# Kernel optimization log

Measured on AMD Instinct MI355X. Metric: run time of the kernel, lower is better.

## Reference

```python
import jax, jax.numpy as jnp
import numpy as np

SLIDING_WINDOW = 512
LOGIT_SOFTCAP = 50.0
NEG_INF = -1e30


def setup_inputs() -> dict:
    key = jax.random.key(0)
    ks = jax.random.split(key, 3)
    B, S, H, KVH, D, BS = 4, 1024, 32, 8, 128, 64
    nb = S // BS          # blocks per sequence = 16
    nblocks = B * nb      # total cache blocks = 64
    total = B * S         # flattened tokens = 4096
    return {
        "query": jax.random.normal(ks[0], (total, H, D), dtype=jnp.float32),
        "key": jax.random.normal(ks[1], (total, KVH, D), dtype=jnp.float32),
        "value": jax.random.normal(ks[2], (total, KVH, D), dtype=jnp.float32),
        "k_cache": jnp.zeros((nblocks, BS, KVH, D), dtype=jnp.float32),
        "v_cache": jnp.zeros((nblocks, BS, KVH, D), dtype=jnp.float32),
        "block_offsets": jnp.arange(nblocks, dtype=jnp.int32).reshape(B, nb),
    }


def reference(query, key, value, k_cache, v_cache, block_offsets):
    B, nb = block_offsets.shape
    nblocks, BS, KVH, D = k_cache.shape
    S = nb * BS
    H = query.shape[1]
    G = H // KVH  # GQA group size
    scale = D ** -0.5

    flat_blocks = block_offsets.reshape(-1)  # [B*nb]
    # 1) write new keys/values into the paged cache per the block table
    k_cache = k_cache.at[flat_blocks].set(key.reshape(-1, BS, KVH, D))
    v_cache = v_cache.at[flat_blocks].set(value.reshape(-1, BS, KVH, D))
    # 2) gather per-sequence contiguous K/V from cache blocks
    k = k_cache[flat_blocks].reshape(B, S, KVH, D)
    v = v_cache[flat_blocks].reshape(B, S, KVH, D)

    q = query.reshape(B, S, KVH, G, D)
    scores = jnp.einsum("bqhgd,bkhd->bhgqk", q, k) * scale
    # logit softcapping (Gemma-style)
    scores = jnp.tanh(scores / LOGIT_SOFTCAP) * LOGIT_SOFTCAP
    # causal + sliding-window mask
    i = jnp.arange(S)[:, None]
    j = jnp.arange(S)[None, :]
    mask = (j <= i) & ((i - j) < SLIDING_WINDOW)
    scores = jnp.where(mask, scores, NEG_INF)
    p = jax.nn.softmax(scores, axis=-1)
    out = jnp.einsum("bhgqk,bkhd->bqhgd", p, v)
    return out.reshape(B * S, H, D)
```

## Files before the change

kernel.cpp:

```cpp
#include <hip/hip_runtime.h>
#include <hip/hip_bf16.h>

typedef __bf16 bf16_t;
typedef bf16_t bf16x8 __attribute__((ext_vector_type(8)));
typedef bf16_t bf16x4 __attribute__((ext_vector_type(4)));
typedef float f32x4 __attribute__((ext_vector_type(4)));

#define B_   4
#define S_   1024
#define H_   32
#define KVH_ 8
#define D_   128
#define WIN_ 512
#define KVD_ (KVH_ * D_)
#define LOG2E_ 1.4426950408889634f
#define C1_ (2.0f * (0.08838834764831845f / 50.0f) * LOG2E_)
#define K2_ (50.0f * LOG2E_)
#define EXP2F_(x) __builtin_amdgcn_exp2f(x)

__device__ __forceinline__ void async16(const bf16_t* g, bf16_t* l) {
  __builtin_amdgcn_global_load_lds(
      (const __attribute__((address_space(1))) void*)g,
      (__attribute__((address_space(3))) void*)l, 16, 0, 0);
}

__global__ __launch_bounds__(256) void prep_kv(
    const float* __restrict__ K, const float* __restrict__ V,
    bf16_t* __restrict__ Kb, bf16_t* __restrict__ Vt)
{
  const int j0  = blockIdx.x * 64;
  const int kvh = blockIdx.y;
  const int b   = blockIdx.z;
  const int t   = threadIdx.x;
  const int j   = t >> 2;
  const int d0  = (t & 3) * 32;
  __shared__ bf16_t tl[128][72];

  {
    const float* src = K + (size_t)(b * S_ + j0 + j) * KVD_ + kvh * D_ + d0;
    bf16_t* dst = Kb + ((size_t)(b * KVH_ + kvh) * S_ + j0 + j) * D_ + d0;
    #pragma unroll
    for (int c = 0; c < 4; ++c) {
      float4 f0 = *(const float4*)(src + c * 8);
      float4 f1 = *(const float4*)(src + c * 8 + 4);
      bf16x8 o = { (bf16_t)f0.x, (bf16_t)f0.y, (bf16_t)f0.z, (bf16_t)f0.w,
                   (bf16_t)f1.x, (bf16_t)f1.y, (bf16_t)f1.z, (bf16_t)f1.w };
      *(bf16x8*)(dst + c * 8) = o;
    }
  }
  {
    const float* src = V + (size_t)(b * S_ + j0 + j) * KVD_ + kvh * D_ + d0;
    #pragma unroll
    for (int c = 0; c < 8; ++c) {
      float4 f = *(const float4*)(src + c * 4);
      tl[d0 + c * 4 + 0][j] = (bf16_t)f.x;
      tl[d0 + c * 4 + 1][j] = (bf16_t)f.y;
      tl[d0 + c * 4 + 2][j] = (bf16_t)f.z;
      tl[d0 + c * 4 + 3][j] = (bf16_t)f.w;
    }
  }
  __syncthreads();
  {
    const int d = t >> 1, half = (t & 1) * 32;
    bf16_t* dst = Vt + ((size_t)(b * KVH_ + kvh) * D_ + d) * S_ + j0 + half;
    #pragma unroll
    for (int c = 0; c < 4; ++c)
      *(bf16x8*)(dst + c * 8) = *(bf16x8*)&tl[d][half + c * 8];
  }
}

__global__ __launch_bounds__(512, 2) void attn_fwd(
    const float* __restrict__ Q, const bf16_t* __restrict__ Kb,
    const bf16_t* __restrict__ Vt, float* __restrict__ Out)
{
  const int i0  = blockIdx.x * 32;
  const int kvh = blockIdx.y;
  const int b   = blockIdx.z;

  const int tid  = threadIdx.x;
  const int w    = tid >> 6;
  const int lane = tid & 63;
  const int m16  = lane & 15;
  const int quad = lane >> 4;
  const int g    = w & 3;
  const int rb   = w >> 2;
  const int h    = kvh * 4 + g;
  const int iw   = i0 + rb * 16;
  const int i    = iw + m16;

  __shared__ __align__(16) bf16_t KsB[2][64 * 128];
  __shared__ __align__(16) bf16_t VtB[2][128 * 64];
  __shared__ __align__(16) bf16_t PsB[8 * 16 * 64];

  bf16x8 qf[4];
  {
    const float* qp = Q + ((size_t)(b * S_ + iw + m16) * H_ + h) * D_;
    #pragma unroll
    for (int s = 0; s < 4; ++s) {
      const int d0 = 32 * s + 8 * quad;
      float4 f0 = *(const float4*)(qp + d0);
      float4 f1 = *(const float4*)(qp + d0 + 4);
      bf16x8 t = { (bf16_t)f0.x, (bf16_t)f0.y, (bf16_t)f0.z, (bf16_t)f0.w,
                   (bf16_t)f1.x, (bf16_t)f1.y, (bf16_t)f1.z, (bf16_t)f1.w };
      qf[s] = t;
    }
  }

  f32x4 O[8];
  #pragma unroll
  for (int c = 0; c < 8; ++c) O[c] = (f32x4){0.f, 0.f, 0.f, 0.f};
  float m_run = -1e30f, l_run = 0.f;

  const bf16_t* khead = Kb + (size_t)(b * KVH_ + kvh) * S_ * D_;
  const bf16_t* vhead = Vt + (size_t)(b * KVH_ + kvh) * D_ * S_;

  const int t_lo = (i0 >= WIN_) ? ((i0 - (WIN_ - 1)) >> 6) : 0;
  const int t_hi = i0 >> 6;

  auto stage = [&](int j0v, int bi) {
    #pragma unroll
    for (int q = 0; q < 2; ++q) {
      const int c   = w * 128 + q * 64 + lane;
      const int krow = c >> 4, kpos = c & 15;
      async16(khead + (size_t)(j0v + krow) * D_ + (((kpos ^ (krow & 15))) << 3),
              &KsB[bi][(w * 128 + q * 64) * 8]);
      const int vd = c >> 3, vpos = c & 7;
      async16(vhead + (size_t)vd * S_ + j0v + (((vpos ^ (vd & 7))) << 3),
              &VtB[bi][(w * 128 + q * 64) * 8]);
    }
  };

  stage(t_lo * 64, 0);
  int buf = 0;

  for (int tb = t_lo; tb <= t_hi; ++tb) {
    const int j0 = tb * 64;
    __syncthreads();
    if (tb < t_hi) stage(j0 + 64, buf ^ 1);

    if (!(j0 > iw + 15 || j0 + 63 < iw - (WIN_ - 1))) {
      f32x4 st[4];
      #pragma unroll
      for (int t4 = 0; t4 < 4; ++t4) {
        f32x4 acc = (f32x4){0.f, 0.f, 0.f, 0.f};
        const int row = 16 * t4 + m16;
        #pragma unroll
        for (int s = 0; s < 4; ++s) {
          bf16x8 a = *(const bf16x8*)&KsB[buf][row * 128 + (((quad + 4 * s) ^ m16) << 3)];
          acc = __builtin_amdgcn_mfma_f32_16x16x32_bf16(a, qf[s], acc, 0, 0, 0);
        }
        st[t4] = acc;
      }

      const bool full = (j0 + 63 <= iw) && (iw + 15 - j0 < WIN_);
      float vmax = -1e30f;
      if (full) {
        #pragma unroll
        for (int t4 = 0; t4 < 4; ++t4)
          #pragma unroll
          for (int r = 0; r < 4; ++r) {
            float ez  = EXP2F_(st[t4][r] * C1_);
            float cap = K2_ * (ez - 1.f) * __builtin_amdgcn_rcpf(ez + 1.f);
            st[t4][r] = cap;
            vmax = fmaxf(vmax, cap);
          }
      } else {
        #pragma unroll
        for (int t4 = 0; t4 < 4; ++t4)
          #pragma unroll
          for (int r = 0; r < 4; ++r) {
            const int j = j0 + t4 * 16 + 4 * quad + r;
            const bool valid = (j <= i) && (i - j < WIN_);
            float ez  = EXP2F_(st[t4][r] * C1_);
            float cap = K2_ * (ez - 1.f) * __builtin_amdgcn_rcpf(ez + 1.f);
            float sm  = valid ? cap : -1e30f;
            st[t4][r] = sm;
            vmax = fmaxf(vmax, sm);
          }
      }
      vmax = fmaxf(vmax, __shfl_xor(vmax, 16));
      vmax = fmaxf(vmax, __shfl_xor(vmax, 32));
      const float m_new = fmaxf(m_run, vmax);
      const float alpha = EXP2F_(m_run - m_new);

      float rs = 0.f;
      if (full) {
        #pragma unroll
        for (int t4 = 0; t4 < 4; ++t4)
          #pragma unroll
          for (int r = 0; r < 4; ++r) {
            float p = EXP2F_(st[t4][r] - m_new);
            st[t4][r] = p; rs += p;
          }
      } else {
        #pragma unroll
        for (int t4 = 0; t4 < 4; ++t4)
          #pragma unroll
          for (int r = 0; r < 4; ++r) {
            const int j = j0 + t4 * 16 + 4 * quad + r;
            const bool valid = (j <= i) && (i - j < WIN_);
            float p = valid ? EXP2F_(st[t4][r] - m_new) : 0.f;
            st[t4][r] = p; rs += p;
          }
      }
      rs += __shfl_xor(rs, 16);
      rs += __shfl_xor(rs, 32);
      l_run = l_run * alpha + rs;
      m_run = m_new;

      const int pw = w * (16 * 64);
      #pragma unroll
      for (int t4 = 0; t4 < 4; ++t4) {
        bf16x4 pk = { (bf16_t)st[t4][0], (bf16_t)st[t4][1],
                      (bf16_t)st[t4][2], (bf16_t)st[t4][3] };
        const int ch = (2 * t4 + (quad >> 1)) ^ (m16 & 7);
        *(bf16x4*)&PsB[pw + m16 * 64 + ch * 8 + (quad & 1) * 4] = pk;
      }
      bf16x8 pa0 = *(const bf16x8*)&PsB[pw + m16 * 64 + (((quad)     ^ (m16 & 7)) << 3)];
      bf16x8 pa1 = *(const bf16x8*)&PsB[pw + m16 * 64 + (((quad + 4) ^ (m16 & 7)) << 3)];

      if (__ballot(alpha != 1.0f)) {
        #pragma unroll
        for (int r = 0; r < 4; ++r) {
          const float ar = __shfl(alpha, 4 * quad + r);
          #pragma unroll
          for (int c = 0; c < 8; ++c) O[c][r] *= ar;
        }
      }

      #pragma unroll
      for (int c = 0; c < 8; ++c) {
        const int row = (16 * c + m16) * 64;
        bf16x8 v0 = *(const bf16x8*)&VtB[buf][row + (((quad)     ^ (m16 & 7)) << 3)];
        bf16x8 v1 = *(const bf16x8*)&VtB[buf][row + (((quad + 4) ^ (m16 & 7)) << 3)];
        O[c] = __builtin_amdgcn_mfma_f32_16x16x32_bf16(pa0, v0, O[c], 0, 0, 0);
        O[c] = __builtin_amdgcn_mfma_f32_16x16x32_bf16(pa1, v1, O[c], 0, 0, 0);
      }
    }
    buf ^= 1;
  }

  float* ob = Out + ((size_t)(b * S_ + iw) * H_ + h) * D_;
  #pragma unroll
  for (int r = 0; r < 4; ++r) {
    const int rr = 4 * quad + r;
    const float lr = __shfl(l_run, rr);
    const float linv = __builtin_amdgcn_rcpf(lr);
    float* po = ob + (size_t)rr * (H_ * D_);
    #pragma unroll
    for (int c = 0; c < 8; ++c) po[c * 16 + m16] = O[c][r] * linv;
  }
}

extern "C" void kernel_launch(void* const* d_in, const int* in_sizes, int n_in,
                              void* d_out, int out_size, void* d_ws, size_t ws_size,
                              hipStream_t stream) {
  const float* q = (const float*)d_in[0];
  const float* k = (const float*)d_in[1];
  const float* v = (const float*)d_in[2];
  float* out = (float*)d_out;
  const size_t nkv = (size_t)B_ * KVH_ * S_ * D_;
  bf16_t *kb, *vt;
  if (ws_size >= 2 * nkv * sizeof(bf16_t)) {
    kb = (bf16_t*)d_ws; vt = kb + nkv;
  } else {
    kb = (bf16_t*)d_in[3]; vt = (bf16_t*)d_in[4];
  }
  prep_kv<<<dim3(S_ / 64, KVH_, B_), 256, 0, stream>>>(k, v, kb, vt);
  attn_fwd<<<dim3(S_ / 32, KVH_, B_), 512, 0, stream>>>(q, kb, vt, out);
}
```

Measured before the change: 257.0 us.

## Drop online softmax max tracking using softcap bound; shrink KV tile to 32

Because softcapping bounds every score to at most 50, the kernel drops the running max, rescaling and the shuffle reductions. It computes p = exp(cap - 50) directly as exp2(-2*K2/(e+1)), which folds the tanh into a single exponential. The KV tile shrinks from 64 to 32 rows and staging moves from async global-to-LDS loads to register prefetch plus an LDS store. Launch bounds go to 6 blocks and a block-index swizzle groups tiles. The fixed offset gives up the numerical safety of the running max, though the bounded range keeps it stable, and the smaller tiles double the number of loop iterations and barriers.

```diff
diff --git a/kernel.cpp b/kernel.cpp
--- a/kernel.cpp
+++ b/kernel.cpp
@@ -16,13 +16,8 @@
 #define LOG2E_ 1.4426950408889634f
 #define C1_ (2.0f * (0.08838834764831845f / 50.0f) * LOG2E_)
 #define K2_ (50.0f * LOG2E_)
+#define NK22_ (-2.0f * K2_)
 #define EXP2F_(x) __builtin_amdgcn_exp2f(x)
-
-__device__ __forceinline__ void async16(const bf16_t* g, bf16_t* l) {
-  __builtin_amdgcn_global_load_lds(
-      (const __attribute__((address_space(1))) void*)g,
-      (__attribute__((address_space(3))) void*)l, 16, 0, 0);
-}
 
 __global__ __launch_bounds__(256) void prep_kv(
     const float* __restrict__ K, const float* __restrict__ V,
@@ -69,13 +64,15 @@
   }
 }
 
-__global__ __launch_bounds__(512, 2) void attn_fwd(
+__global__ __launch_bounds__(512, 6) void attn_fwd(
     const float* __restrict__ Q, const bf16_t* __restrict__ Kb,
     const bf16_t* __restrict__ Vt, float* __restrict__ Out)
 {
-  const int i0  = blockIdx.x * 32;
-  const int kvh = blockIdx.y;
-  const int b   = blockIdx.z;
+  const int fid = blockIdx.x + 32 * (blockIdx.y + 8 * (int)blockIdx.z);
+  const int swz = (fid & 7) * 128 + (fid >> 3);
+  const int i0  = (swz & 31) * 32;
+  const int kvh = (swz >> 5) & 7;
+  const int b   = swz >> 8;
 
   const int tid  = threadIdx.x;
   const int w    = tid >> 6;
@@ -88,9 +85,9 @@
   const int iw   = i0 + rb * 16;
   const int i    = iw + m16;
 
-  __shared__ __align__(16) bf16_t KsB[2][64 * 128];
-  __shared__ __align__(16) bf16_t VtB[2][128 * 64];
-  __shared__ __align__(16) bf16_t PsB[8 * 16 * 64];
+  __shared__ __align__(16) bf16_t KsB[2][32 * 128];
+  __shared__ __align__(16) bf16_t VtB[2][128 * 32];
+  __shared__ __align__(16) bf16_t PsB[8 * 16 * 32];
 
   bf16x8 qf[4];
   {
@@ -109,39 +106,45 @@
   f32x4 O[8];
   #pragma unroll
   for (int c = 0; c < 8; ++c) O[c] = (f32x4){0.f, 0.f, 0.f, 0.f};
-  float m_run = -1e30f, l_run = 0.f;
+  f32x4 lacc = (f32x4){0.f, 0.f, 0.f, 0.f};
 
   const bf16_t* khead = Kb + (size_t)(b * KVH_ + kvh) * S_ * D_;
   const bf16_t* vhead = Vt + (size_t)(b * KVH_ + kvh) * D_ * S_;
 
-  const int t_lo = (i0 >= WIN_) ? ((i0 - (WIN_ - 1)) >> 6) : 0;
-  const int t_hi = i0 >> 6;
-
-  auto stage = [&](int j0v, int bi) {
-    #pragma unroll
-    for (int q = 0; q < 2; ++q) {
-      const int c   = w * 128 + q * 64 + lane;
-      const int krow = c >> 4, kpos = c & 15;
-      async16(khead + (size_t)(j0v + krow) * D_ + (((kpos ^ (krow & 15))) << 3),
-              &KsB[bi][(w * 128 + q * 64) * 8]);
-      const int vd = c >> 3, vpos = c & 7;
-      async16(vhead + (size_t)vd * S_ + j0v + (((vpos ^ (vd & 7))) << 3),
-              &VtB[bi][(w * 128 + q * 64) * 8]);
-    }
-  };
-
-  stage(t_lo * 64, 0);
+  const int krow = tid >> 4, kpos = tid & 15;
+  const int vd   = tid >> 2, vpos = tid & 3;
+  const bf16_t* ksrc = khead + (size_t)krow * D_ + kpos * 8;
+  const bf16_t* vsrc = vhead + (size_t)vd * S_ + vpos * 8;
+  const int koff = krow * 128 + ((kpos ^ (krow & 15)) << 3);
+  const int voff = vd * 32 + ((vpos ^ (vd & 3)) << 3);
+
+  const int t_lo = (i0 >= WIN_) ? ((i0 - (WIN_ - 1)) >> 5) : 0;
+  const int t_hi = i0 >> 5;
+
+  {
+    int4 kr = *(const int4*)(ksrc + (size_t)t_lo * 32 * D_);
+    int4 vr = *(const int4*)(vsrc + t_lo * 32);
+    *(int4*)&KsB[0][koff] = kr;
+    *(int4*)&VtB[0][voff] = vr;
+  }
+  __syncthreads();
   int buf = 0;
 
   for (int tb = t_lo; tb <= t_hi; ++tb) {
-    const int j0 = tb * 64;
-    __syncthreads();
-    if (tb < t_hi) stage(j0 + 64, buf ^ 1);
-
-    if (!(j0 > iw + 15 || j0 + 63 < iw - (WIN_ - 1))) {
-      f32x4 st[4];
+    const int j0  = tb * 32;
+    const bool pre = (tb < t_hi);
+    int4 kr, vr;
+    if (pre) {
+      kr = *(const int4*)(ksrc + (size_t)(j0 + 32) * D_);
+      vr = *(const int4*)(vsrc + (j0 + 32));
+    }
+
+    if (!(j0 > iw + 15 || j0 + 31 < iw - (WIN_ - 1))) {
+      const bool full = (j0 + 31 <= iw) && (iw + 15 - j0 < WIN_);
+      const int pw = w * (16 * 32);
+
       #pragma unroll
-      for (int t4 = 0; t4 < 4; ++t4) {
+      for (int t4 = 0; t4 < 2; ++t4) {
         f32x4 acc = (f32x4){0.f, 0.f, 0.f, 0.f};
         const int row = 16 * t4 + m16;
         #pragma unroll
@@ -149,96 +152,42 @@
           bf16x8 a = *(const bf16x8*)&KsB[buf][row * 128 + (((quad + 4 * s) ^ m16) << 3)];
           acc = __builtin_amdgcn_mfma_f32_16x16x32_bf16(a, qf[s], acc, 0, 0, 0);
         }
-        st[t4] = acc;
-      }
-
-      const bool full = (j0 + 63 <= iw) && (iw + 15 - j0 < WIN_);
-      float vmax = -1e30f;
-      if (full) {
-        #pragma unroll
-        for (int t4 = 0; t4 < 4; ++t4)
-          #pragma unroll
-          for (int r = 0; r < 4; ++r) {
-            float ez  = EXP2F_(st[t4][r] * C1_);
-            float cap = K2_ * (ez - 1.f) * __builtin_amdgcn_rcpf(ez + 1.f);
-            st[t4][r] = cap;
-            vmax = fmaxf(vmax, cap);
-          }
-      } else {
-        #pragma unroll
-        for (int t4 = 0; t4 < 4; ++t4)
-          #pragma unroll
-          for (int r = 0; r < 4; ++r) {
-            const int j = j0 + t4 * 16 + 4 * quad + r;
-            const bool valid = (j <= i) && (i - j < WIN_);
-            float ez  = EXP2F_(st[t4][r] * C1_);
-            float cap = K2_ * (ez - 1.f) * __builtin_amdgcn_rcpf(ez + 1.f);
-            float sm  = valid ? cap : -1e30f;
-            st[t4][r] = sm;
-            vmax = fmaxf(vmax, sm);
-          }
-      }
-      vmax = fmaxf(vmax, __shfl_xor(vmax, 16));
-      vmax = fmaxf(vmax, __shfl_xor(vmax, 32));
-      const float m_new = fmaxf(m_run, vmax);
-      const float alpha = EXP2F_(m_run - m_new);
-
-      float rs = 0.f;
-      if (full) {
-        #pragma unroll
-        for (int t4 = 0; t4 < 4; ++t4)
-          #pragma unroll
-          for (int r = 0; r < 4; ++r) {
-            float p = EXP2F_(st[t4][r] - m_new);
-            st[t4][r] = p; rs += p;
-          }
-      } else {
-        #pragma unroll
-        for (int t4 = 0; t4 < 4; ++t4)
-          #pragma unroll
-          for (int r = 0; r < 4; ++r) {
-            const int j = j0 + t4 * 16 + 4 * quad + r;
-            const bool valid = (j <= i) && (i - j < WIN_);
-            float p = valid ? EXP2F_(st[t4][r] - m_new) : 0.f;
-            st[t4][r] = p; rs += p;
-          }
-      }
-      rs += __shfl_xor(rs, 16);
-      rs += __shfl_xor(rs, 32);
-      l_run = l_run * alpha + rs;
-      m_run = m_new;
-
-      const int pw = w * (16 * 64);
-      #pragma unroll
-      for (int t4 = 0; t4 < 4; ++t4) {
-        bf16x4 pk = { (bf16_t)st[t4][0], (bf16_t)st[t4][1],
-                      (bf16_t)st[t4][2], (bf16_t)st[t4][3] };
-        const int ch = (2 * t4 + (quad >> 1)) ^ (m16 & 7);
-        *(bf16x4*)&PsB[pw + m16 * 64 + ch * 8 + (quad & 1) * 4] = pk;
-      }
-      bf16x8 pa0 = *(const bf16x8*)&PsB[pw + m16 * 64 + (((quad)     ^ (m16 & 7)) << 3)];
-      bf16x8 pa1 = *(const bf16x8*)&PsB[pw + m16 * 64 + (((quad + 4) ^ (m16 & 7)) << 3)];
-
-      if (__ballot(alpha != 1.0f)) {
+        bf16x4 pk;
         #pragma unroll
         for (int r = 0; r < 4; ++r) {
-          const float ar = __shfl(alpha, 4 * quad + r);
-          #pragma unroll
-          for (int c = 0; c < 8; ++c) O[c][r] *= ar;
+          float ez = EXP2F_(acc[r] * C1_);
+          float p  = EXP2F_(NK22_ * __builtin_amdgcn_rcpf(ez + 1.f));
+          if (!full) {
+            const int j = j0 + t4 * 16 + 4 * quad + r;
+            p = ((j <= i) && (i - j < WIN_)) ? p : 0.f;
+          }
+          lacc[r] += p;
+          pk[r] = (bf16_t)p;
         }
+        const int ch = (2 * t4 + (quad >> 1)) ^ (m16 & 3);
+        *(bf16x4*)&PsB[pw + m16 * 32 + ch * 8 + (quad & 1) * 4] = pk;
       }
+      bf16x8 pa = *(const bf16x8*)&PsB[pw + m16 * 32 + ((quad ^ (m16 & 3)) << 3)];
 
       #pragma unroll
       for (int c = 0; c < 8; ++c) {
-        const int row = (16 * c + m16) * 64;
-        bf16x8 v0 = *(const bf16x8*)&VtB[buf][row + (((quad)     ^ (m16 & 7)) << 3)];
-        bf16x8 v1 = *(const bf16x8*)&VtB[buf][row + (((quad + 4) ^ (m16 & 7)) << 3)];
-        O[c] = __builtin_amdgcn_mfma_f32_16x16x32_bf16(pa0, v0, O[c], 0, 0, 0);
-        O[c] = __builtin_amdgcn_mfma_f32_16x16x32_bf16(pa1, v1, O[c], 0, 0, 0);
+        const int vrow = 16 * c + m16;
+        bf16x8 v = *(const bf16x8*)&VtB[buf][vrow * 32 + ((quad ^ (m16 & 3)) << 3)];
+        O[c] = __builtin_amdgcn_mfma_f32_16x16x32_bf16(pa, v, O[c], 0, 0, 0);
       }
     }
+
+    if (pre) {
+      *(int4*)&KsB[buf ^ 1][koff] = kr;
+      *(int4*)&VtB[buf ^ 1][voff] = vr;
+    }
+    __syncthreads();
     buf ^= 1;
   }
+
+  float l_run = lacc[0] + lacc[1] + lacc[2] + lacc[3];
+  l_run += __shfl_xor(l_run, 16);
+  l_run += __shfl_xor(l_run, 32);
 
   float* ob = Out + ((size_t)(b * S_ + iw) * H_ + h) * D_;
   #pragma unroll
```

Result: slower. 301.5 us (+17.3%).
